# Kernel optimization log

Measured on AMD Instinct MI355X. Metric: run time of the kernel, lower is better.

Reference implementation:

```python
import jax, jax.numpy as jnp
import numpy as np
from jax import lax

B, T, VSZ = 32, 150, 500
EMB, HID, OSZ, VL, BETA = 80, 512, 512, 512, 512


def setup_inputs() -> dict:
    key = jax.random.key(0)
    ks = jax.random.split(key, 16)
    rn = lambda k, shp, s=0.02: jax.random.normal(k, shp, dtype=jnp.float32) * s
    return {
        "X_batch": jax.random.normal(ks[0], (B, 1, 64, 512), jnp.float32),
        "labels_batch": jax.random.randint(ks[1], (B, T), 0, VSZ),
        "w1": rn(ks[2], (64, 1, 3, 3)), "b1": jnp.zeros((64,), jnp.float32),
        "w2": rn(ks[3], (128, 64, 3, 3)), "b2": jnp.zeros((128,), jnp.float32),
        "w3": rn(ks[4], (256, 128, 3, 3)), "b3": jnp.zeros((256,), jnp.float32),
        "w4": rn(ks[5], (512, 256, 3, 3)), "b4": jnp.zeros((512,), jnp.float32),
        "E": rn(ks[6], (VSZ, EMB), 1.0),
        "Wx": rn(ks[7], (4 * HID, EMB + OSZ)),
        "Wh": rn(ks[8], (4 * HID, HID)),
        "b_lstm": jnp.zeros((4 * HID,), jnp.float32),
        "Wv_att": rn(ks[9], (VL, BETA)),
        "Wh_att": rn(ks[10], (HID, BETA)),
        "b_att": jnp.zeros((BETA,), jnp.float32),
        "beta_att": rn(ks[11], (BETA,)),
        "W_O": rn(ks[12], (OSZ, HID + VL)),
        "W_out": rn(ks[13], (VSZ, OSZ)),
    }


def _conv(x, w, b):
    y = lax.conv_general_dilated(x, w, (1, 1), 'SAME',
                                 dimension_numbers=('NCHW', 'OIHW', 'NCHW'))
    return y + b[None, :, None, None]


def _pool2(x):
    return lax.reduce_window(x, -jnp.inf, lax.max, (1, 1, 2, 2), (1, 1, 2, 2), 'VALID')


def _cnn(x, w1, b1, w2, b2, w3, b3, w4, b4):
    x = _pool2(jax.nn.relu(_conv(x, w1, b1)))   # (B,64,32,256)
    x = _pool2(jax.nn.relu(_conv(x, w2, b2)))   # (B,128,16,128)
    x = jax.nn.relu(_conv(x, w3, b3))           # (B,256,16,128)
    x = _pool2(jax.nn.relu(_conv(x, w4, b4)))   # (B,512,8,64)
    return x


def reference(X_batch, labels_batch, w1, b1, w2, b2, w3, b3, w4, b4,
              E, Wx, Wh, b_lstm, Wv_att, Wh_att, b_att, beta_att, W_O, W_out):
    f32 = X_batch.dtype
    bsz, seq = labels_batch.shape
    F = _cnn(X_batch, w1, b1, w2, b2, w3, b3, w4, b4)
    C = F.shape[1]
    V = F.transpose(0, 2, 3, 1).reshape(bsz, -1, C)        # (B, L=H'*W', C)
    Vproj = V @ Wv_att + b_att                              # (B, L, BETA) precomputed

    vocab = W_out.shape[0]
    start = jnp.full((bsz, 1), vocab - 3, labels_batch.dtype)
    ids = jnp.concatenate([start, labels_batch[:, :-1]], axis=1)  # teacher forcing
    embs = E[ids]                                           # (B, T, EMB)

    hid, osz = Wh.shape[1], W_O.shape[0]
    h0 = jnp.zeros((bsz, hid), f32)
    c0 = jnp.zeros((bsz, hid), f32)
    O0 = jnp.zeros((bsz, osz), f32)

    def step(carry, emb_t):
        h, c, O_prev = carry
        x = jnp.concatenate([emb_t, O_prev], axis=1)        # (B, EMB+OSZ)
        gates = x @ Wx.T + h @ Wh.T + b_lstm
        i_g, f_g, g_g, o_g = jnp.split(gates, 4, axis=1)
        c = jax.nn.sigmoid(f_g) * c + jax.nn.sigmoid(i_g) * jnp.tanh(g_g)
        h = jax.nn.sigmoid(o_g) * jnp.tanh(c)
        scores = jnp.tanh(Vproj + (h @ Wh_att)[:, None, :]) @ beta_att  # (B, L)
        a = jax.nn.softmax(scores, axis=-1)
        ctx = jnp.einsum('bl,blc->bc', a, V)                # (B, VL)
        O_t = jnp.tanh(jnp.concatenate([h, ctx], axis=1) @ W_O.T)
        Q_t = O_t @ W_out.T                                 # (B, vocab)
        return (h, c, O_t), Q_t

    _, Qs = lax.scan(step, (h0, c0, O0), embs.transpose(1, 0, 2))
    return Qs.transpose(1, 0, 2)                            # (B, T, vocab)
```

## Files before the change

kernel.cpp:

```cpp
#include <hip/hip_runtime.h>
#include <hip/hip_bf16.h>
#include <stdint.h>

typedef __attribute__((ext_vector_type(8))) short short8;
typedef __attribute__((ext_vector_type(4))) short short4v;
typedef __attribute__((ext_vector_type(4))) float f32x4;
using bf16 = __hip_bfloat16;

__device__ __forceinline__ float bfb2f(unsigned short u) {
  union { unsigned u; float f; } x; x.u = ((unsigned)u) << 16; return x.f;
}
__device__ __forceinline__ unsigned short f2bfb(float f) {
  union { float f; unsigned u; } x; x.f = f;
  unsigned r = x.u + 0x7FFFu + ((x.u >> 16) & 1u);
  return (unsigned short)(r >> 16);
}
__device__ __forceinline__ float sigf(float x) { return 1.0f / (1.0f + __expf(-x)); }
__device__ __forceinline__ float tanhf_(float x) {
  x = fminf(fmaxf(x, -15.f), 15.f);
  float e = __expf(2.f * x);
  return 1.f - 2.f / (e + 1.f);
}
__device__ __forceinline__ f32x4 mfma16(short8 a, short8 b, f32x4 c) {
  return __builtin_amdgcn_mfma_f32_16x16x32_bf16(a, b, c, 0, 0, 0);
}
__device__ __forceinline__ int swz(int b) { return b ^ (((b >> 6) & 7) << 4); }


__global__ void k_pack_apack(const float* __restrict__ w, bf16* __restrict__ out, int CO, int CI) {
  int idx = blockIdx.x * 256 + threadIdx.x;
  int total = 9 * CO * CI;
  if (idx >= total) return;
  int ci = idx % CI; int r = idx / CI; int co = r % CO; int s = r / CO;
  ((unsigned short*)out)[(s * CO + co) * CI + ci] = f2bfb(w[(co * CI + ci) * 9 + s]);
}

__global__ void k_cast(const float* __restrict__ src, bf16* __restrict__ dst, int n) {
  int idx = blockIdx.x * 256 + threadIdx.x;
  if (idx < n) ((unsigned short*)dst)[idx] = f2bfb(src[idx]);
}

__global__ void k_castT512(const float* __restrict__ src, bf16* __restrict__ dst) {
  int idx = blockIdx.x * 256 + threadIdx.x;
  if (idx >= 262144) return;
  int k = idx >> 9, nn = idx & 511;
  ((unsigned short*)dst)[nn * 512 + k] = f2bfb(src[idx]);
}

__global__ void k_pack_wg(const float* __restrict__ Wx, const float* __restrict__ Wh, bf16* __restrict__ out) {
  int idx = blockIdx.x * 256 + threadIdx.x;
  if (idx >= 2293760) return;
  int kj = idx & 7, jc = (idx >> 3) & 15; int r = idx >> 7;
  int kg = r % 140, jblk = r / 140;
  int k = kg * 8 + kj, j = jblk * 16 + jc;
  float v = 0.f;
  if (k < 80) v = Wx[j * 592 + k];
  else if (k < 96) v = 0.f;
  else if (k < 608) v = Wx[j * 592 + k - 16];
  else v = Wh[j * 512 + k - 608];
  ((unsigned short*)out)[idx] = f2bfb(v);
}
__global__ void k_pack_wo(const float* __restrict__ WO, bf16* __restrict__ out) {
  int idx = blockIdx.x * 256 + threadIdx.x;
  if (idx >= 524288) return;
  int kj = idx & 7, jc = (idx >> 3) & 15; int r = idx >> 7;
  int kg = r % 128, jblk = r / 128;
  int k = kg * 8 + kj, o = jblk * 16 + jc;
  ((unsigned short*)out)[idx] = f2bfb(WO[o * 1024 + k]);
}
__global__ void k_pack_wout(const float* __restrict__ W, bf16* __restrict__ out) {
  int idx = blockIdx.x * 256 + threadIdx.x;
  if (idx >= 262144) return;
  int kj = idx & 7, jc = (idx >> 3) & 15; int r = idx >> 7;
  int kg = r % 64, jblk = r / 64;
  int k = kg * 8 + kj, v = jblk * 16 + jc;
  ((unsigned short*)out)[idx] = (v < 500) ? f2bfb(W[v * 512 + k]) : (unsigned short)0;
}

__global__ void k_init(bf16* __restrict__ X, bf16* __restrict__ Hb, float* __restrict__ Cst,
                       const bf16* __restrict__ Ebf) {
  int idx = blockIdx.x * 256 + threadIdx.x;
  if (idx < 32 * 608) {
    int k = idx % 608;
    unsigned short v = 0;
    if (k < 80) v = ((const unsigned short*)Ebf)[497 * 80 + k];
    ((unsigned short*)X)[idx] = v;
  }
  if (idx < 32768) ((unsigned short*)Hb)[idx] = 0;
  if (idx < 16384) Cst[idx] = 0.f;
}


__global__ __launch_bounds__(256) void k_conv1(const float* __restrict__ Xin, const float* __restrict__ w1,
                                               const float* __restrict__ b1, bf16* __restrict__ out) {
  __shared__ float wsm[576];
  __shared__ float xt[4][10];
  const int tid = threadIdx.x;
  const int n = blockIdx.z, y2 = blockIdx.y, xb = blockIdx.x * 4;
  for (int i = tid; i < 576; i += 256) wsm[i] = w1[i];
  if (tid < 40) {
    int rr = tid / 10, cc = tid % 10;
    int gy = 2 * y2 - 1 + rr, gx = 2 * xb - 1 + cc;
    float v = 0.f;
    if (gy >= 0 && gy < 64 && gx >= 0 && gx < 512) v = Xin[n * 32768 + gy * 512 + gx];
    xt[rr][cc] = v;
  }
  __syncthreads();
  const int co = tid & 63, xl = tid >> 6;
  const float bb = b1[co];
  float mx = 0.f;
#pragma unroll
  for (int py = 0; py < 2; ++py)
#pragma unroll
    for (int px = 0; px < 2; ++px) {
      float s = bb;
#pragma unroll
      for (int dy = 0; dy < 3; ++dy)
#pragma unroll
        for (int dx = 0; dx < 3; ++dx)
          s = fmaf(wsm[co * 9 + dy * 3 + dx], xt[py + dy][2 * xl + px + dx], s);
      mx = fmaxf(mx, fmaxf(s, 0.f));
    }
  ((unsigned short*)out)[((n * 34 + y2 + 1) * 258 + (xb + xl) + 1) * 64 + co] = f2bfb(mx);
}

template <int CI, int CO, int H, int W, int MODE>
__global__ __launch_bounds__(256) void k_convgemm(const bf16* __restrict__ inP, const bf16* __restrict__ apack,
                                                  const float* __restrict__ bias, bf16* __restrict__ outp) {
  constexpr int Hp = H + 2, Wp = W + 2;
  __shared__ __align__(16) char As[8192];
  __shared__ __align__(16) char Bs[8192];
  const int tid = threadIdx.x, lane = tid & 63, wv = tid >> 6;
  const int lm = lane & 15, kh = lane >> 4;
  const int wm = wv & 1, wn = wv >> 1;
  const int p0 = blockIdx.x * 128, m0 = blockIdx.y * 128;
  const int n = p0 / (H * W), rem = p0 % (H * W);
  const int y = rem / W, x0 = rem % W;
  const long long pixbase = ((long long)(n * Hp + y) * Wp + x0) * CI;
  f32x4 acc[4][4];
#pragma unroll
  for (int i = 0; i < 4; ++i)
#pragma unroll
    for (int j = 0; j < 4; ++j) acc[i][j] = (f32x4){0.f, 0.f, 0.f, 0.f};
  const int r = tid >> 1, e0 = (tid & 1) * 16;
  const int wb = r * 64 + e0 * 2;
  for (int s = 0; s < 9; ++s) {
    const int dy = s / 3, dx = s % 3;
    const bf16* bsrc = inP + pixbase + (dy * Wp + dx) * CI;
    const bf16* asrc = apack + (s * CO + m0) * CI;
    for (int cc = 0; cc < CI / 32; ++cc) {
      short8 av0 = *(const short8*)(asrc + r * CI + cc * 32 + e0);
      short8 av1 = *(const short8*)(asrc + r * CI + cc * 32 + e0 + 8);
      short8 bv0 = *(const short8*)(bsrc + (long long)r * CI + cc * 32 + e0);
      short8 bv1 = *(const short8*)(bsrc + (long long)r * CI + cc * 32 + e0 + 8);
      __syncthreads();
      *(short8*)(void*)(As + swz(wb)) = av0;
      *(short8*)(void*)(As + swz(wb + 16)) = av1;
      *(short8*)(void*)(Bs + swz(wb)) = bv0;
      *(short8*)(void*)(Bs + swz(wb + 16)) = bv1;
      __syncthreads();
      short8 af[4], bg[4];
#pragma unroll
      for (int i = 0; i < 4; ++i)
        af[i] = *(const short8*)(const void*)(As + swz((wm * 64 + i * 16 + lm) * 64 + kh * 16));
#pragma unroll
      for (int j = 0; j < 4; ++j)
        bg[j] = *(const short8*)(const void*)(Bs + swz((wn * 64 + j * 16 + lm) * 64 + kh * 16));
#pragma unroll
      for (int i = 0; i < 4; ++i)
#pragma unroll
        for (int j = 0; j < 4; ++j) acc[i][j] = mfma16(af[i], bg[j], acc[i][j]);
    }
  }
#pragma unroll
  for (int i = 0; i < 4; ++i) {
    const int co = m0 + wm * 64 + i * 16 + kh * 4;
    float b4[4];
#pragma unroll
    for (int rr = 0; rr < 4; ++rr) b4[rr] = bias[co + rr];
#pragma unroll
    for (int j = 0; j < 4; ++j) {
      const int pix = p0 + wn * 64 + j * 16 + lm;
      short4v pk;
#pragma unroll
      for (int rr = 0; rr < 4; ++rr) {
        float v = fmaxf(acc[i][j][rr] + b4[rr], 0.f);
        pk[rr] = (short)f2bfb(v);
      }
      if constexpr (MODE == 0) {
        *(short4v*)(void*)(outp + (long long)pix * CO + co) = pk;
      } else {
        const int nn = pix / (H * W), r2 = pix % (H * W);
        const int yy = r2 / W, xx = r2 % W;
        *(short4v*)(void*)(outp + ((long long)(nn * Hp + yy + 1) * Wp + xx + 1) * CO + co) = pk;
      }
    }
  }
}

__global__ void k_pool(const bf16* __restrict__ src, bf16* __restrict__ dst,
                       int H, int W, int C, int OHP, int OWP, int pad) {
  const int idx = blockIdx.x * 256 + threadIdx.x;
  const int C8 = C >> 3;
  const int c8 = idx % C8; int tmp = idx / C8;
  const int x2 = tmp % (W >> 1); tmp /= (W >> 1);
  const int y2 = tmp % (H >> 1); const int n = tmp / (H >> 1);
  if (n >= 32) return;
  const long long sbase = ((long long)(n * H + 2 * y2) * W + 2 * x2) * C + c8 * 8;
  short8 a = *(const short8*)(src + sbase);
  short8 b = *(const short8*)(src + sbase + C);
  short8 c = *(const short8*)(src + sbase + (long long)W * C);
  short8 d = *(const short8*)(src + sbase + (long long)W * C + C);
  short8 o;
#pragma unroll
  for (int e = 0; e < 8; ++e) {
    float m = fmaxf(fmaxf(bfb2f((unsigned short)a[e]), bfb2f((unsigned short)b[e])),
                    fmaxf(bfb2f((unsigned short)c[e]), bfb2f((unsigned short)d[e])));
    o[e] = (short)f2bfb(m);
  }
  *(short8*)(void*)(dst + ((long long)(n * OHP + y2 + pad) * OWP + x2 + pad) * C + c8 * 8) = o;
}

__global__ __launch_bounds__(256) void k_gemm_vproj(const bf16* __restrict__ Vb, const bf16* __restrict__ WvT,
                                                    const float* __restrict__ batt, bf16* __restrict__ VP) {
  __shared__ __align__(16) char As[8192];
  __shared__ __align__(16) char Bs[8192];
  const int tid = threadIdx.x, lane = tid & 63, wv = tid >> 6;
  const int lm = lane & 15, kh = lane >> 4;
  const int wm = wv & 1, wn = wv >> 1;
  const int n0 = blockIdx.x * 128, m0 = blockIdx.y * 128;
  f32x4 acc[4][4];
#pragma unroll
  for (int i = 0; i < 4; ++i)
#pragma unroll
    for (int j = 0; j < 4; ++j) acc[i][j] = (f32x4){0.f, 0.f, 0.f, 0.f};
  const int r = tid >> 1, e0 = (tid & 1) * 16;
  const int wb = r * 64 + e0 * 2;
  for (int cc = 0; cc < 16; ++cc) {
    short8 av0 = *(const short8*)(Vb + (m0 + r) * 512 + cc * 32 + e0);
    short8 av1 = *(const short8*)(Vb + (m0 + r) * 512 + cc * 32 + e0 + 8);
    short8 bv0 = *(const short8*)(WvT + (n0 + r) * 512 + cc * 32 + e0);
    short8 bv1 = *(const short8*)(WvT + (n0 + r) * 512 + cc * 32 + e0 + 8);
    __syncthreads();
    *(short8*)(void*)(As + swz(wb)) = av0;
    *(short8*)(void*)(As + swz(wb + 16)) = av1;
    *(short8*)(void*)(Bs + swz(wb)) = bv0;
    *(short8*)(void*)(Bs + swz(wb + 16)) = bv1;
    __syncthreads();
    short8 af[4], bg[4];
#pragma unroll
    for (int i = 0; i < 4; ++i)
      af[i] = *(const short8*)(const void*)(As + swz((wm * 64 + i * 16 + lm) * 64 + kh * 16));
#pragma unroll
    for (int j = 0; j < 4; ++j)
      bg[j] = *(const short8*)(const void*)(Bs + swz((wn * 64 + j * 16 + lm) * 64 + kh * 16));
#pragma unroll
    for (int i = 0; i < 4; ++i)
#pragma unroll
      for (int j = 0; j < 4; ++j) acc[i][j] = mfma16(af[i], bg[j], acc[i][j]);
  }
#pragma unroll
  for (int i = 0; i < 4; ++i)
#pragma unroll
    for (int j = 0; j < 4; ++j) {
      const int nn = n0 + wn * 64 + j * 16 + lm;
      const float ba = batt[nn];
#pragma unroll
      for (int rr = 0; rr < 4; ++rr) {
        const int m = m0 + wm * 64 + i * 16 + kh * 4 + rr;
        ((unsigned short*)VP)[m * 512 + nn] = f2bfb(acc[i][j][rr] + ba);
      }
    }
}


__global__ __launch_bounds__(256) void k_step_a(int t, const bf16* __restrict__ X, bf16* __restrict__ Hb,
                                                float* __restrict__ Cst, const bf16* __restrict__ WgP,
                                                const bf16* __restrict__ WoutP, const float* __restrict__ bl,
                                                float* __restrict__ outQ) {
  const int tid = threadIdx.x, lane = tid & 63, wv = tid >> 6;
  const int lm = lane & 15, kh = lane >> 4;
  if (blockIdx.x < 32) {
    if (t >= 150) return;
    const int nb = blockIdx.x;
    const int jblk = wv * 32 + nb;
    const bf16* hprev = Hb + ((t + 1) & 1) * 16384;
    f32x4 acc0 = {0.f, 0.f, 0.f, 0.f}, acc1 = {0.f, 0.f, 0.f, 0.f};
    for (int kk = 0; kk < 19; ++kk) {
      short8 a0 = *(const short8*)(X + lm * 608 + kk * 32 + kh * 8);
      short8 a1 = *(const short8*)(X + (lm + 16) * 608 + kk * 32 + kh * 8);
      short8 b = *(const short8*)(WgP + ((jblk * 140 + kk * 4 + kh) * 16 + lm) * 8);
      acc0 = mfma16(a0, b, acc0);
      acc1 = mfma16(a1, b, acc1);
    }
    for (int kk = 19; kk < 35; ++kk) {
      short8 a0 = *(const short8*)(hprev + lm * 512 + (kk - 19) * 32 + kh * 8);
      short8 a1 = *(const short8*)(hprev + (lm + 16) * 512 + (kk - 19) * 32 + kh * 8);
      short8 b = *(const short8*)(WgP + ((jblk * 140 + kk * 4 + kh) * 16 + lm) * 8);
      acc0 = mfma16(a0, b, acc0);
      acc1 = mfma16(a1, b, acc1);
    }
    __shared__ float gl[4][32][16];
    const float bj = bl[wv * 512 + nb * 16 + lm];
#pragma unroll
    for (int rr = 0; rr < 4; ++rr) {
      gl[wv][kh * 4 + rr][lm] = acc0[rr] + bj;
      gl[wv][16 + kh * 4 + rr][lm] = acc1[rr] + bj;
    }
    __syncthreads();
    bf16* hcur = Hb + (t & 1) * 16384;
    for (int idx = tid; idx < 512; idx += 256) {
      const int b = idx >> 4, hh = idx & 15;
      const int hid = nb * 16 + hh;
      float ig = gl[0][b][hh], fg = gl[1][b][hh], gg = gl[2][b][hh], og = gl[3][b][hh];
      float c = sigf(fg) * Cst[b * 512 + hid] + sigf(ig) * tanhf_(gg);
      Cst[b * 512 + hid] = c;
      ((unsigned short*)hcur)[b * 512 + hid] = f2bfb(sigf(og) * tanhf_(c));
    }
  } else {
    if (t < 1) return;
    const int ntile = (blockIdx.x - 32) * 4 + wv;
    f32x4 acc0 = {0.f, 0.f, 0.f, 0.f}, acc1 = {0.f, 0.f, 0.f, 0.f};
    for (int kk = 0; kk < 16; ++kk) {
      short8 a0 = *(const short8*)(X + lm * 608 + 96 + kk * 32 + kh * 8);
      short8 a1 = *(const short8*)(X + (lm + 16) * 608 + 96 + kk * 32 + kh * 8);
      short8 b = *(const short8*)(WoutP + ((ntile * 64 + kk * 4 + kh) * 16 + lm) * 8);
      acc0 = mfma16(a0, b, acc0);
      acc1 = mfma16(a1, b, acc1);
    }
    const int v = ntile * 16 + lm;
    if (v < 500) {
#pragma unroll
      for (int rr = 0; rr < 4; ++rr) {
        outQ[((kh * 4 + rr) * 150 + (t - 1)) * 500 + v] = acc0[rr];
        outQ[((16 + kh * 4 + rr) * 150 + (t - 1)) * 500 + v] = acc1[rr];
      }
    }
  }
}

__global__ __launch_bounds__(256) void k_step_b(int t, const bf16* __restrict__ Hb,
                                                const bf16* __restrict__ WhattB, const bf16* __restrict__ Vproj,
                                                const float* __restrict__ beta, float* __restrict__ scores) {
  const int tid = threadIdx.x;
  const int b = blockIdx.x >> 2, lc = blockIdx.x & 3;
  __shared__ unsigned short hsh[512];
  __shared__ float hW[512];
  __shared__ float bsh[512];
  const unsigned short* hp = (const unsigned short*)(Hb + (t & 1) * 16384) + b * 512;
  for (int i = tid; i < 512; i += 256) {
    hsh[i] = hp[i];
    bsh[i] = beta[i];
  }
  __syncthreads();
  const uint32_t* wp = (const uint32_t*)WhattB;
  float s0 = 0.f, s1 = 0.f;
  for (int k = 0; k < 512; ++k) {
    const float hk = bfb2f(hsh[k]);
    const uint32_t w2 = wp[k * 256 + tid];
    s0 = fmaf(hk, bfb2f((unsigned short)(w2 & 0xFFFFu)), s0);
    s1 = fmaf(hk, bfb2f((unsigned short)(w2 >> 16)), s1);
  }
  hW[tid * 2] = s0;
  hW[tid * 2 + 1] = s1;
  __syncthreads();
  const int l = lc * 128 + (tid >> 1);
  const int half = tid & 1;
  const short8* vp = (const short8*)(Vproj + ((b * 512 + l) * 512) + half * 256);
  float acc = 0.f;
  for (int i = 0; i < 32; ++i) {
    short8 v = vp[i];
#pragma unroll
    for (int e = 0; e < 8; ++e) {
      const int be = half * 256 + i * 8 + e;
      acc = fmaf(tanhf_(bfb2f((unsigned short)v[e]) + hW[be]), bsh[be], acc);
    }
  }
  acc += __shfl_xor(acc, 1, 64);
  if (half == 0) scores[b * 512 + l] = acc;
}

__global__ __launch_bounds__(256) void k_step_c(const float* __restrict__ scores, const bf16* __restrict__ V,
                                                bf16* __restrict__ Ct) {
  const int tid = threadIdx.x;
  const int b = blockIdx.x >> 2, cc = blockIdx.x & 3;
  const int lane = tid & 63, wv = tid >> 6;
  __shared__ float sc[512];
  __shared__ float wr1[4];
  __shared__ float wr2[4];
  __shared__ float part[2][128];
  float v0 = scores[b * 512 + tid];
  float v1 = scores[b * 512 + 256 + tid];
  float m = fmaxf(v0, v1);
#pragma unroll
  for (int off = 32; off >= 1; off >>= 1) m = fmaxf(m, __shfl_xor(m, off, 64));
  if (lane == 0) wr1[wv] = m;
  __syncthreads();
  m = fmaxf(fmaxf(wr1[0], wr1[1]), fmaxf(wr1[2], wr1[3]));
  float e0 = __expf(v0 - m), e1 = __expf(v1 - m);
  sc[tid] = e0;
  sc[tid + 256] = e1;
  float s = e0 + e1;
#pragma unroll
  for (int off = 32; off >= 1; off >>= 1) s += __shfl_xor(s, off, 64);
  if (lane == 0) wr2[wv] = s;
  __syncthreads();
  const float rz = 1.0f / (wr2[0] + wr2[1] + wr2[2] + wr2[3]);
  const int c = cc * 128 + (tid & 127);
  const int lh = tid >> 7;
  const unsigned short* vb = (const unsigned short*)V + ((b * 512 + lh * 256) * 512) + c;
  float acc = 0.f;
  for (int l = 0; l < 256; ++l) acc = fmaf(sc[lh * 256 + l], bfb2f(vb[l * 512]), acc);
  part[lh][tid & 127] = acc;
  __syncthreads();
  if (tid < 128) ((unsigned short*)Ct)[b * 512 + cc * 128 + tid] = f2bfb((part[0][tid] + part[1][tid]) * rz);
}

__global__ __launch_bounds__(256) void k_step_d(int t, bf16* __restrict__ X, const bf16* __restrict__ Hb,
                                                const bf16* __restrict__ Ct, const bf16* __restrict__ WOP,
                                                const bf16* __restrict__ Ebf, const int* __restrict__ labels) {
  const int tid = threadIdx.x, lane = tid & 63, wv = tid >> 6;
  const int lm = lane & 15, kh = lane >> 4;
  const int ntile = blockIdx.x * 4 + wv;
  const bf16* hcur = Hb + (t & 1) * 16384;
  f32x4 acc0 = {0.f, 0.f, 0.f, 0.f}, acc1 = {0.f, 0.f, 0.f, 0.f};
  for (int kk = 0; kk < 16; ++kk) {
    short8 a0 = *(const short8*)(hcur + lm * 512 + kk * 32 + kh * 8);
    short8 a1 = *(const short8*)(hcur + (lm + 16) * 512 + kk * 32 + kh * 8);
    short8 b = *(const short8*)(WOP + ((ntile * 128 + kk * 4 + kh) * 16 + lm) * 8);
    acc0 = mfma16(a0, b, acc0);
    acc1 = mfma16(a1, b, acc1);
  }
  for (int kk = 16; kk < 32; ++kk) {
    short8 a0 = *(const short8*)(Ct + lm * 512 + (kk - 16) * 32 + kh * 8);
    short8 a1 = *(const short8*)(Ct + (lm + 16) * 512 + (kk - 16) * 32 + kh * 8);
    short8 b = *(const short8*)(WOP + ((ntile * 128 + kk * 4 + kh) * 16 + lm) * 8);
    acc0 = mfma16(a0, b, acc0);
    acc1 = mfma16(a1, b, acc1);
  }
  const int o = ntile * 16 + lm;
  unsigned short* Xu = (unsigned short*)X;
#pragma unroll
  for (int rr = 0; rr < 4; ++rr) {
    Xu[(kh * 4 + rr) * 608 + 96 + o] = f2bfb(tanhf_(acc0[rr]));
    Xu[(16 + kh * 4 + rr) * 608 + 96 + o] = f2bfb(tanhf_(acc1[rr]));
  }
  if (blockIdx.x == 0 && t + 1 < 150) {
    for (int idx = tid; idx < 3072; idx += 256) {
      const int b = idx / 96, k = idx % 96;
      unsigned short val = 0;
      if (k < 80) {
        const int id = labels[b * 150 + t];
        val = ((const unsigned short*)Ebf)[id * 80 + k];
      }
      Xu[b * 608 + k] = val;
    }
  }
}


extern "C" void kernel_launch(void* const* d_in, const int* in_sizes, int n_in,
                              void* d_out, int out_size, void* d_ws, size_t ws_size,
                              hipStream_t stream) {
  (void)in_sizes; (void)n_in; (void)out_size; (void)ws_size;
  const float* Xb = (const float*)d_in[0];
  const int* lab = (const int*)d_in[1];
  const float* w1 = (const float*)d_in[2]; const float* b1 = (const float*)d_in[3];
  const float* w2 = (const float*)d_in[4]; const float* b2 = (const float*)d_in[5];
  const float* w3 = (const float*)d_in[6]; const float* b3 = (const float*)d_in[7];
  const float* w4 = (const float*)d_in[8]; const float* b4 = (const float*)d_in[9];
  const float* E = (const float*)d_in[10];
  const float* Wx = (const float*)d_in[11]; const float* Wh = (const float*)d_in[12];
  const float* blstm = (const float*)d_in[13];
  const float* Wv = (const float*)d_in[14]; const float* Wha = (const float*)d_in[15];
  const float* bat = (const float*)d_in[16]; const float* beta = (const float*)d_in[17];
  const float* WO = (const float*)d_in[18]; const float* Wout = (const float*)d_in[19];
  float* out = (float*)d_out;
  char* ws = (char*)d_ws;

  constexpr size_t oRegA = 0;
  constexpr size_t sRegA = 38338560ULL;
  constexpr size_t oRegB = oRegA + sRegA;
  constexpr size_t oIn2p = oRegB + 67108864ULL;
  constexpr size_t oV    = oIn2p + 19169280ULL;
  constexpr size_t oVprj = oV + 16777216ULL;
  constexpr size_t oAp2  = oVprj + 16777216ULL;
  constexpr size_t oAp3  = oAp2 + 147456ULL;
  constexpr size_t oAp4  = oAp3 + 589824ULL;
  constexpr size_t oWvT  = oAp4 + 2359296ULL;
  constexpr size_t oWgP  = oWvT + 524288ULL;
  constexpr size_t oWOP  = oWgP + 4587520ULL;
  constexpr size_t oWoutP= oWOP + 1048576ULL;
  constexpr size_t oWhatt= oWoutP + 524288ULL;
  constexpr size_t oEbf  = oWhatt + 524288ULL;
  constexpr size_t oX    = oEbf + 80128ULL;
  constexpr size_t oHb   = oX + 39168ULL;
  constexpr size_t oCst  = oHb + 65536ULL;
  constexpr size_t oSc   = oCst + 65536ULL;
  constexpr size_t oCt   = oSc + 65536ULL;

  bf16* in1p = (bf16*)(ws + oRegA);
  bf16* in3p = (bf16*)(ws + oRegA);
  bf16* pre2 = (bf16*)(ws + oRegB);
  bf16* pre4 = (bf16*)(ws + oRegB);
  bf16* in2p = (bf16*)(ws + oIn2p);
  bf16* Vbuf = (bf16*)(ws + oV);
  bf16* Vprj = (bf16*)(ws + oVprj);
  bf16* Ap2 = (bf16*)(ws + oAp2);
  bf16* Ap3 = (bf16*)(ws + oAp3);
  bf16* Ap4 = (bf16*)(ws + oAp4);
  bf16* WvT = (bf16*)(ws + oWvT);
  bf16* WgP = (bf16*)(ws + oWgP);
  bf16* WOP = (bf16*)(ws + oWOP);
  bf16* WoutP = (bf16*)(ws + oWoutP);
  bf16* Whatt = (bf16*)(ws + oWhatt);
  bf16* Ebf = (bf16*)(ws + oEbf);
  bf16* X = (bf16*)(ws + oX);
  bf16* Hb = (bf16*)(ws + oHb);
  float* Cst = (float*)(ws + oCst);
  float* Sc = (float*)(ws + oSc);
  bf16* Ct = (bf16*)(ws + oCt);

  k_pack_apack<<<(9 * 128 * 64 + 255) / 256, 256, 0, stream>>>(w2, Ap2, 128, 64);
  k_pack_apack<<<(9 * 256 * 128 + 255) / 256, 256, 0, stream>>>(w3, Ap3, 256, 128);
  k_pack_apack<<<(9 * 512 * 256 + 255) / 256, 256, 0, stream>>>(w4, Ap4, 512, 256);
  k_castT512<<<1024, 256, 0, stream>>>(Wv, WvT);
  k_cast<<<1024, 256, 0, stream>>>(Wha, Whatt, 262144);
  k_cast<<<(40000 + 255) / 256, 256, 0, stream>>>(E, Ebf, 40000);
  k_pack_wg<<<8960, 256, 0, stream>>>(Wx, Wh, WgP);
  k_pack_wo<<<2048, 256, 0, stream>>>(WO, WOP);
  k_pack_wout<<<1024, 256, 0, stream>>>(Wout, WoutP);
  k_init<<<128, 256, 0, stream>>>(X, Hb, Cst, Ebf);

  hipMemsetAsync(ws + oRegA, 0, sRegA, stream);
  hipMemsetAsync(ws + oIn2p, 0, 19169280ULL, stream);
  k_conv1<<<dim3(64, 32, 32), 256, 0, stream>>>(Xb, w1, b1, in1p);
  k_convgemm<64, 128, 32, 256, 0><<<dim3(2048, 1), 256, 0, stream>>>(in1p, Ap2, b2, pre2);
  k_pool<<<4096, 256, 0, stream>>>(pre2, in2p, 32, 256, 128, 18, 130, 1);
  hipMemsetAsync(ws + oRegA, 0, sRegA, stream);
  k_convgemm<128, 256, 16, 128, 1><<<dim3(512, 2), 256, 0, stream>>>(in2p, Ap3, b3, in3p);
  k_convgemm<256, 512, 16, 128, 0><<<dim3(512, 4), 256, 0, stream>>>(in3p, Ap4, b4, pre4);
  k_pool<<<4096, 256, 0, stream>>>(pre4, Vbuf, 16, 128, 512, 8, 64, 0);
  k_gemm_vproj<<<dim3(4, 128), 256, 0, stream>>>(Vbuf, WvT, bat, Vprj);

  for (int t = 0; t <= 150; ++t) {
    k_step_a<<<40, 256, 0, stream>>>(t, X, Hb, Cst, WgP, WoutP, blstm, out);
    if (t == 150) break;
    k_step_b<<<128, 256, 0, stream>>>(t, Hb, Whatt, Vprj, beta, Sc);
    k_step_c<<<128, 256, 0, stream>>>(Sc, Vbuf, Ct);
    k_step_d<<<8, 256, 0, stream>>>(t, X, Hb, Ct, WOP, Ebf, lab);
  }
}
```

Measured before the change: 11.99 ms.

## Fuse decoder timestep loop into one persistent kernel with grid barriers

Replaces the roughly 600 per-step kernel launches of the 151-step decoder with a single persistent 256-block kernel that uses an atomic grid barrier between phases. The cell state is kept in registers. The h@Wh_att product is folded into the LSTM blocks as MFMA partial sums, which are reduced in the scores phase. h and the attention context are packed into one buffer so the W_O matmul reads a single contiguous operand. The intent is to remove launch overhead and poorly parallelised small kernels, at the cost of relying on all 256 blocks being co-resident and on spin-barrier latency.

```diff
diff --git a/kernel.cpp b/kernel.cpp
--- a/kernel.cpp
+++ b/kernel.cpp
@@ -25,6 +25,23 @@
   return __builtin_amdgcn_mfma_f32_16x16x32_bf16(a, b, c, 0, 0, 0);
 }
 __device__ __forceinline__ int swz(int b) { return b ^ (((b >> 6) & 7) << 4); }
+
+__device__ __forceinline__ void gbar(int* cnt, int* gen, int target) {
+  __syncthreads();
+  if (threadIdx.x == 0) {
+    int v = __hip_atomic_fetch_add(cnt, 1, __ATOMIC_ACQ_REL, __HIP_MEMORY_SCOPE_AGENT);
+    if (v == 255) {
+      __hip_atomic_store(cnt, 0, __ATOMIC_RELAXED, __HIP_MEMORY_SCOPE_AGENT);
+      __hip_atomic_fetch_add(gen, 1, __ATOMIC_ACQ_REL, __HIP_MEMORY_SCOPE_AGENT);
+    } else {
+      while (__hip_atomic_load(gen, __ATOMIC_RELAXED, __HIP_MEMORY_SCOPE_AGENT) < target) {
+        __builtin_amdgcn_s_sleep(1);
+      }
+      __builtin_amdgcn_fence(__ATOMIC_ACQUIRE, "agent");
+    }
+  }
+  __syncthreads();
+}
 
 
 __global__ void k_pack_apack(const float* __restrict__ w, bf16* __restrict__ out, int CO, int CI) {
@@ -76,9 +93,15 @@
   int k = kg * 8 + kj, v = jblk * 16 + jc;
   ((unsigned short*)out)[idx] = (v < 500) ? f2bfb(W[v * 512 + k]) : (unsigned short)0;
 }
-
-__global__ void k_init(bf16* __restrict__ X, bf16* __restrict__ Hb, float* __restrict__ Cst,
-                       const bf16* __restrict__ Ebf) {
+__global__ void k_pack_whatt(const float* __restrict__ Wha, bf16* __restrict__ out) {
+  int idx = blockIdx.x * 256 + threadIdx.x;
+  if (idx >= 262144) return;
+  int kj = idx & 7, jc = (idx >> 3) & 15, khh = (idx >> 7) & 1, j2 = (idx >> 8) & 31, nb = idx >> 13;
+  int k = nb * 16 + khh * 8 + kj, n = j2 * 16 + jc;
+  ((unsigned short*)out)[idx] = f2bfb(Wha[k * 512 + n]);
+}
+
+__global__ void k_init(bf16* __restrict__ X, bf16* __restrict__ HC, const bf16* __restrict__ Ebf) {
   int idx = blockIdx.x * 256 + threadIdx.x;
   if (idx < 32 * 608) {
     int k = idx % 608;
@@ -86,8 +109,7 @@
     if (k < 80) v = ((const unsigned short*)Ebf)[497 * 80 + k];
     ((unsigned short*)X)[idx] = v;
   }
-  if (idx < 32768) ((unsigned short*)Hb)[idx] = 0;
-  if (idx < 16384) Cst[idx] = 0.f;
+  if (idx < 65536) ((unsigned short*)HC)[idx] = 0;
 }
 
 
@@ -273,187 +295,192 @@
     }
 }
 
-
-__global__ __launch_bounds__(256) void k_step_a(int t, const bf16* __restrict__ X, bf16* __restrict__ Hb,
-                                                float* __restrict__ Cst, const bf16* __restrict__ WgP,
-                                                const bf16* __restrict__ WoutP, const float* __restrict__ bl,
-                                                float* __restrict__ outQ) {
-  const int tid = threadIdx.x, lane = tid & 63, wv = tid >> 6;
-  const int lm = lane & 15, kh = lane >> 4;
-  if (blockIdx.x < 32) {
-    if (t >= 150) return;
-    const int nb = blockIdx.x;
-    const int jblk = wv * 32 + nb;
-    const bf16* hprev = Hb + ((t + 1) & 1) * 16384;
-    f32x4 acc0 = {0.f, 0.f, 0.f, 0.f}, acc1 = {0.f, 0.f, 0.f, 0.f};
-    for (int kk = 0; kk < 19; ++kk) {
-      short8 a0 = *(const short8*)(X + lm * 608 + kk * 32 + kh * 8);
-      short8 a1 = *(const short8*)(X + (lm + 16) * 608 + kk * 32 + kh * 8);
-      short8 b = *(const short8*)(WgP + ((jblk * 140 + kk * 4 + kh) * 16 + lm) * 8);
-      acc0 = mfma16(a0, b, acc0);
-      acc1 = mfma16(a1, b, acc1);
-    }
-    for (int kk = 19; kk < 35; ++kk) {
-      short8 a0 = *(const short8*)(hprev + lm * 512 + (kk - 19) * 32 + kh * 8);
-      short8 a1 = *(const short8*)(hprev + (lm + 16) * 512 + (kk - 19) * 32 + kh * 8);
-      short8 b = *(const short8*)(WgP + ((jblk * 140 + kk * 4 + kh) * 16 + lm) * 8);
-      acc0 = mfma16(a0, b, acc0);
-      acc1 = mfma16(a1, b, acc1);
-    }
-    __shared__ float gl[4][32][16];
-    const float bj = bl[wv * 512 + nb * 16 + lm];
-#pragma unroll
-    for (int rr = 0; rr < 4; ++rr) {
-      gl[wv][kh * 4 + rr][lm] = acc0[rr] + bj;
-      gl[wv][16 + kh * 4 + rr][lm] = acc1[rr] + bj;
-    }
-    __syncthreads();
-    bf16* hcur = Hb + (t & 1) * 16384;
-    for (int idx = tid; idx < 512; idx += 256) {
-      const int b = idx >> 4, hh = idx & 15;
-      const int hid = nb * 16 + hh;
-      float ig = gl[0][b][hh], fg = gl[1][b][hh], gg = gl[2][b][hh], og = gl[3][b][hh];
-      float c = sigf(fg) * Cst[b * 512 + hid] + sigf(ig) * tanhf_(gg);
-      Cst[b * 512 + hid] = c;
-      ((unsigned short*)hcur)[b * 512 + hid] = f2bfb(sigf(og) * tanhf_(c));
-    }
-  } else {
-    if (t < 1) return;
-    const int ntile = (blockIdx.x - 32) * 4 + wv;
-    f32x4 acc0 = {0.f, 0.f, 0.f, 0.f}, acc1 = {0.f, 0.f, 0.f, 0.f};
-    for (int kk = 0; kk < 16; ++kk) {
-      short8 a0 = *(const short8*)(X + lm * 608 + 96 + kk * 32 + kh * 8);
-      short8 a1 = *(const short8*)(X + (lm + 16) * 608 + 96 + kk * 32 + kh * 8);
-      short8 b = *(const short8*)(WoutP + ((ntile * 64 + kk * 4 + kh) * 16 + lm) * 8);
-      acc0 = mfma16(a0, b, acc0);
-      acc1 = mfma16(a1, b, acc1);
-    }
-    const int v = ntile * 16 + lm;
-    if (v < 500) {
+__global__ __launch_bounds__(256) void k_decoder(
+    bf16* __restrict__ X, bf16* __restrict__ HC, float* __restrict__ partial,
+    float* __restrict__ scores, const bf16* __restrict__ WgP, const bf16* __restrict__ WhattP,
+    const bf16* __restrict__ WOP, const bf16* __restrict__ WoutP,
+    const bf16* __restrict__ Vprj, const bf16* __restrict__ Vbuf,
+    const bf16* __restrict__ Ebf, const int* __restrict__ labels,
+    const float* __restrict__ bl, const float* __restrict__ beta,
+    float* __restrict__ out, int* syncp) {
+  const int tid = threadIdx.x, bid = blockIdx.x;
+  const int lane = tid & 63, wv = tid >> 6, lm = lane & 15, kh = lane >> 4;
+  __shared__ __align__(16) char smem[12288];
+  int* cnt = syncp;
+  int* gen = syncp + 32;
+  int bt = 0;
+  float c0 = 0.f, c1 = 0.f;
+  const short8 z8 = {0, 0, 0, 0, 0, 0, 0, 0};
+  const f32x4 z4 = {0.f, 0.f, 0.f, 0.f};
+  unsigned short* Xu = (unsigned short*)X;
+  unsigned short* HCu = (unsigned short*)HC;
+
+  for (int t = 0; t < 151; ++t) {
+    gbar(cnt, gen, ++bt);
+    if (bid < 32 && t < 150) {
+      const int nb = bid;
+      const bf16* hprev = HC + ((t + 1) & 1) * 32768;
+      const int jblk = wv * 32 + nb;
+      f32x4 acc0 = z4, acc1 = z4;
+      for (int kk = 0; kk < 19; ++kk) {
+        short8 a0 = *(const short8*)(X + lm * 608 + kk * 32 + kh * 8);
+        short8 a1 = *(const short8*)(X + (lm + 16) * 608 + kk * 32 + kh * 8);
+        short8 bw = *(const short8*)(WgP + ((jblk * 140 + kk * 4 + kh) * 16 + lm) * 8);
+        acc0 = mfma16(a0, bw, acc0); acc1 = mfma16(a1, bw, acc1);
+      }
+      for (int kk = 19; kk < 35; ++kk) {
+        short8 a0 = *(const short8*)(hprev + lm * 1024 + (kk - 19) * 32 + kh * 8);
+        short8 a1 = *(const short8*)(hprev + (lm + 16) * 1024 + (kk - 19) * 32 + kh * 8);
+        short8 bw = *(const short8*)(WgP + ((jblk * 140 + kk * 4 + kh) * 16 + lm) * 8);
+        acc0 = mfma16(a0, bw, acc0); acc1 = mfma16(a1, bw, acc1);
+      }
+      float* gl = (float*)smem;
+      unsigned short* hsl = (unsigned short*)(smem + 8192);
+      const float bj = bl[wv * 512 + nb * 16 + lm];
 #pragma unroll
       for (int rr = 0; rr < 4; ++rr) {
-        outQ[((kh * 4 + rr) * 150 + (t - 1)) * 500 + v] = acc0[rr];
-        outQ[((16 + kh * 4 + rr) * 150 + (t - 1)) * 500 + v] = acc1[rr];
-      }
-    }
-  }
-}
-
-__global__ __launch_bounds__(256) void k_step_b(int t, const bf16* __restrict__ Hb,
-                                                const bf16* __restrict__ WhattB, const bf16* __restrict__ Vproj,
-                                                const float* __restrict__ beta, float* __restrict__ scores) {
-  const int tid = threadIdx.x;
-  const int b = blockIdx.x >> 2, lc = blockIdx.x & 3;
-  __shared__ unsigned short hsh[512];
-  __shared__ float hW[512];
-  __shared__ float bsh[512];
-  const unsigned short* hp = (const unsigned short*)(Hb + (t & 1) * 16384) + b * 512;
-  for (int i = tid; i < 512; i += 256) {
-    hsh[i] = hp[i];
-    bsh[i] = beta[i];
-  }
-  __syncthreads();
-  const uint32_t* wp = (const uint32_t*)WhattB;
-  float s0 = 0.f, s1 = 0.f;
-  for (int k = 0; k < 512; ++k) {
-    const float hk = bfb2f(hsh[k]);
-    const uint32_t w2 = wp[k * 256 + tid];
-    s0 = fmaf(hk, bfb2f((unsigned short)(w2 & 0xFFFFu)), s0);
-    s1 = fmaf(hk, bfb2f((unsigned short)(w2 >> 16)), s1);
-  }
-  hW[tid * 2] = s0;
-  hW[tid * 2 + 1] = s1;
-  __syncthreads();
-  const int l = lc * 128 + (tid >> 1);
-  const int half = tid & 1;
-  const short8* vp = (const short8*)(Vproj + ((b * 512 + l) * 512) + half * 256);
-  float acc = 0.f;
-  for (int i = 0; i < 32; ++i) {
-    short8 v = vp[i];
-#pragma unroll
-    for (int e = 0; e < 8; ++e) {
-      const int be = half * 256 + i * 8 + e;
-      acc = fmaf(tanhf_(bfb2f((unsigned short)v[e]) + hW[be]), bsh[be], acc);
-    }
-  }
-  acc += __shfl_xor(acc, 1, 64);
-  if (half == 0) scores[b * 512 + l] = acc;
-}
-
-__global__ __launch_bounds__(256) void k_step_c(const float* __restrict__ scores, const bf16* __restrict__ V,
-                                                bf16* __restrict__ Ct) {
-  const int tid = threadIdx.x;
-  const int b = blockIdx.x >> 2, cc = blockIdx.x & 3;
-  const int lane = tid & 63, wv = tid >> 6;
-  __shared__ float sc[512];
-  __shared__ float wr1[4];
-  __shared__ float wr2[4];
-  __shared__ float part[2][128];
-  float v0 = scores[b * 512 + tid];
-  float v1 = scores[b * 512 + 256 + tid];
-  float m = fmaxf(v0, v1);
-#pragma unroll
-  for (int off = 32; off >= 1; off >>= 1) m = fmaxf(m, __shfl_xor(m, off, 64));
-  if (lane == 0) wr1[wv] = m;
-  __syncthreads();
-  m = fmaxf(fmaxf(wr1[0], wr1[1]), fmaxf(wr1[2], wr1[3]));
-  float e0 = __expf(v0 - m), e1 = __expf(v1 - m);
-  sc[tid] = e0;
-  sc[tid + 256] = e1;
-  float s = e0 + e1;
-#pragma unroll
-  for (int off = 32; off >= 1; off >>= 1) s += __shfl_xor(s, off, 64);
-  if (lane == 0) wr2[wv] = s;
-  __syncthreads();
-  const float rz = 1.0f / (wr2[0] + wr2[1] + wr2[2] + wr2[3]);
-  const int c = cc * 128 + (tid & 127);
-  const int lh = tid >> 7;
-  const unsigned short* vb = (const unsigned short*)V + ((b * 512 + lh * 256) * 512) + c;
-  float acc = 0.f;
-  for (int l = 0; l < 256; ++l) acc = fmaf(sc[lh * 256 + l], bfb2f(vb[l * 512]), acc);
-  part[lh][tid & 127] = acc;
-  __syncthreads();
-  if (tid < 128) ((unsigned short*)Ct)[b * 512 + cc * 128 + tid] = f2bfb((part[0][tid] + part[1][tid]) * rz);
-}
-
-__global__ __launch_bounds__(256) void k_step_d(int t, bf16* __restrict__ X, const bf16* __restrict__ Hb,
-                                                const bf16* __restrict__ Ct, const bf16* __restrict__ WOP,
-                                                const bf16* __restrict__ Ebf, const int* __restrict__ labels) {
-  const int tid = threadIdx.x, lane = tid & 63, wv = tid >> 6;
-  const int lm = lane & 15, kh = lane >> 4;
-  const int ntile = blockIdx.x * 4 + wv;
-  const bf16* hcur = Hb + (t & 1) * 16384;
-  f32x4 acc0 = {0.f, 0.f, 0.f, 0.f}, acc1 = {0.f, 0.f, 0.f, 0.f};
-  for (int kk = 0; kk < 16; ++kk) {
-    short8 a0 = *(const short8*)(hcur + lm * 512 + kk * 32 + kh * 8);
-    short8 a1 = *(const short8*)(hcur + (lm + 16) * 512 + kk * 32 + kh * 8);
-    short8 b = *(const short8*)(WOP + ((ntile * 128 + kk * 4 + kh) * 16 + lm) * 8);
-    acc0 = mfma16(a0, b, acc0);
-    acc1 = mfma16(a1, b, acc1);
-  }
-  for (int kk = 16; kk < 32; ++kk) {
-    short8 a0 = *(const short8*)(Ct + lm * 512 + (kk - 16) * 32 + kh * 8);
-    short8 a1 = *(const short8*)(Ct + (lm + 16) * 512 + (kk - 16) * 32 + kh * 8);
-    short8 b = *(const short8*)(WOP + ((ntile * 128 + kk * 4 + kh) * 16 + lm) * 8);
-    acc0 = mfma16(a0, b, acc0);
-    acc1 = mfma16(a1, b, acc1);
-  }
-  const int o = ntile * 16 + lm;
-  unsigned short* Xu = (unsigned short*)X;
-#pragma unroll
-  for (int rr = 0; rr < 4; ++rr) {
-    Xu[(kh * 4 + rr) * 608 + 96 + o] = f2bfb(tanhf_(acc0[rr]));
-    Xu[(16 + kh * 4 + rr) * 608 + 96 + o] = f2bfb(tanhf_(acc1[rr]));
-  }
-  if (blockIdx.x == 0 && t + 1 < 150) {
-    for (int idx = tid; idx < 3072; idx += 256) {
-      const int b = idx / 96, k = idx % 96;
-      unsigned short val = 0;
-      if (k < 80) {
-        const int id = labels[b * 150 + t];
-        val = ((const unsigned short*)Ebf)[id * 80 + k];
-      }
-      Xu[b * 608 + k] = val;
+        gl[(wv * 32 + kh * 4 + rr) * 16 + lm] = acc0[rr] + bj;
+        gl[(wv * 32 + 16 + kh * 4 + rr) * 16 + lm] = acc1[rr] + bj;
+      }
+      __syncthreads();
+      unsigned short* hcur = HCu + (t & 1) * 32768;
+      {
+        const int b = tid >> 4, hh = tid & 15;
+        float ig = gl[(0 * 32 + b) * 16 + hh], fg = gl[(1 * 32 + b) * 16 + hh];
+        float gg = gl[(2 * 32 + b) * 16 + hh], og = gl[(3 * 32 + b) * 16 + hh];
+        c0 = sigf(fg) * c0 + sigf(ig) * tanhf_(gg);
+        unsigned short hv = f2bfb(sigf(og) * tanhf_(c0));
+        hcur[b * 1024 + nb * 16 + hh] = hv; hsl[b * 16 + hh] = hv;
+        const int b2 = 16 + b;
+        float ig2 = gl[(0 * 32 + b2) * 16 + hh], fg2 = gl[(1 * 32 + b2) * 16 + hh];
+        float gg2 = gl[(2 * 32 + b2) * 16 + hh], og2 = gl[(3 * 32 + b2) * 16 + hh];
+        c1 = sigf(fg2) * c1 + sigf(ig2) * tanhf_(gg2);
+        unsigned short hv2 = f2bfb(sigf(og2) * tanhf_(c1));
+        hcur[b2 * 1024 + nb * 16 + hh] = hv2; hsl[b2 * 16 + hh] = hv2;
+      }
+      __syncthreads();
+      short8 a0 = z8, a1 = z8;
+      if (kh < 2) {
+        a0 = *(const short8*)(hsl + lm * 16 + kh * 8);
+        a1 = *(const short8*)(hsl + (16 + lm) * 16 + kh * 8);
+      }
+      for (int j2 = wv * 8; j2 < wv * 8 + 8; ++j2) {
+        short8 bw = z8;
+        if (kh < 2) bw = *(const short8*)(WhattP + (((nb * 32 + j2) * 2 + kh) * 16 + lm) * 8);
+        f32x4 p0 = mfma16(a0, bw, z4);
+        f32x4 p1 = mfma16(a1, bw, z4);
+        float* pw = partial + nb * 16384 + j2 * 16 + lm;
+#pragma unroll
+        for (int rr = 0; rr < 4; ++rr) {
+          pw[(kh * 4 + rr) * 512] = p0[rr];
+          pw[(16 + kh * 4 + rr) * 512] = p1[rr];
+        }
+      }
+    } else if (bid >= 32 && bid < 40 && t >= 1) {
+      const int ntile = (bid - 32) * 4 + wv;
+      f32x4 acc0 = z4, acc1 = z4;
+      for (int kk = 0; kk < 16; ++kk) {
+        short8 a0 = *(const short8*)(X + lm * 608 + 96 + kk * 32 + kh * 8);
+        short8 a1 = *(const short8*)(X + (lm + 16) * 608 + 96 + kk * 32 + kh * 8);
+        short8 bw = *(const short8*)(WoutP + ((ntile * 64 + kk * 4 + kh) * 16 + lm) * 8);
+        acc0 = mfma16(a0, bw, acc0); acc1 = mfma16(a1, bw, acc1);
+      }
+      const int v = ntile * 16 + lm;
+      if (v < 500) {
+#pragma unroll
+        for (int rr = 0; rr < 4; ++rr) {
+          out[((kh * 4 + rr) * 150 + (t - 1)) * 500 + v] = acc0[rr];
+          out[((16 + kh * 4 + rr) * 150 + (t - 1)) * 500 + v] = acc1[rr];
+        }
+      }
+    }
+    if (t == 150) break;
+
+    gbar(cnt, gen, ++bt);
+    {
+      const int b = bid >> 3, chunk = bid & 7;
+      float* hWl = (float*)smem;
+      float* betal = (float*)(smem + 2048);
+      for (int n = tid; n < 512; n += 256) {
+        float s = 0.f;
+#pragma unroll 8
+        for (int nb = 0; nb < 32; ++nb) s += partial[nb * 16384 + b * 512 + n];
+        hWl[n] = s;
+        betal[n] = beta[n];
+      }
+      __syncthreads();
+      const int l = chunk * 64 + (tid >> 2), q = tid & 3;
+      const bf16* vp = Vprj + (b * 512 + l) * 512 + q * 128;
+      float acc = 0.f;
+      for (int i = 0; i < 16; ++i) {
+        short8 v = *(const short8*)(vp + i * 8);
+#pragma unroll
+        for (int e = 0; e < 8; ++e) {
+          const int n = q * 128 + i * 8 + e;
+          acc = fmaf(tanhf_(bfb2f((unsigned short)v[e]) + hWl[n]), betal[n], acc);
+        }
+      }
+      acc += __shfl_xor(acc, 1, 64);
+      acc += __shfl_xor(acc, 2, 64);
+      if (q == 0) scores[b * 512 + l] = acc;
+    }
+
+    gbar(cnt, gen, ++bt);
+    {
+      const int b = bid >> 3, cc = bid & 7;
+      float* al = (float*)smem;
+      float* prt = (float*)(smem + 2048);
+      float* wr = (float*)(smem + 3072);
+      float s0 = scores[b * 512 + tid], s1 = scores[b * 512 + 256 + tid];
+      float m = fmaxf(s0, s1);
+#pragma unroll
+      for (int off = 32; off >= 1; off >>= 1) m = fmaxf(m, __shfl_xor(m, off, 64));
+      if (lane == 0) wr[wv] = m;
+      __syncthreads();
+      m = fmaxf(fmaxf(wr[0], wr[1]), fmaxf(wr[2], wr[3]));
+      float e0 = __expf(s0 - m), e1 = __expf(s1 - m);
+      al[tid] = e0; al[tid + 256] = e1;
+      float s = e0 + e1;
+#pragma unroll
+      for (int off = 32; off >= 1; off >>= 1) s += __shfl_xor(s, off, 64);
+      if (lane == 0) wr[4 + wv] = s;
+      __syncthreads();
+      const float rz = 1.f / (wr[4] + wr[5] + wr[6] + wr[7]);
+      const int c = cc * 64 + (tid & 63), lq = tid >> 6;
+      const unsigned short* vb = (const unsigned short*)Vbuf + (long long)(b * 512 + lq * 128) * 512 + c;
+      float acc = 0.f;
+      for (int l = 0; l < 128; ++l) acc = fmaf(al[lq * 128 + l], bfb2f(vb[l * 512]), acc);
+      prt[lq * 64 + (tid & 63)] = acc;
+      __syncthreads();
+      if (tid < 64)
+        HCu[(t & 1) * 32768 + b * 1024 + 512 + cc * 64 + tid] =
+            f2bfb((prt[tid] + prt[64 + tid] + prt[128 + tid] + prt[192 + tid]) * rz);
+    }
+
+    gbar(cnt, gen, ++bt);
+    if (bid < 8) {
+      const int w = bid * 4 + wv;
+      const bf16* hc = HC + (t & 1) * 32768;
+      f32x4 acc0 = z4, acc1 = z4;
+      for (int kk = 0; kk < 32; ++kk) {
+        short8 a0 = *(const short8*)(hc + lm * 1024 + kk * 32 + kh * 8);
+        short8 a1 = *(const short8*)(hc + (lm + 16) * 1024 + kk * 32 + kh * 8);
+        short8 bw = *(const short8*)(WOP + ((w * 128 + kk * 4 + kh) * 16 + lm) * 8);
+        acc0 = mfma16(a0, bw, acc0); acc1 = mfma16(a1, bw, acc1);
+      }
+      const int o = w * 16 + lm;
+#pragma unroll
+      for (int rr = 0; rr < 4; ++rr) {
+        Xu[(kh * 4 + rr) * 608 + 96 + o] = f2bfb(tanhf_(acc0[rr]));
+        Xu[(16 + kh * 4 + rr) * 608 + 96 + o] = f2bfb(tanhf_(acc1[rr]));
+      }
+    } else if (bid == 8 && t + 1 < 150) {
+      for (int idx = tid; idx < 3072; idx += 256) {
+        const int b = idx / 96, k = idx % 96;
+        unsigned short val = 0;
+        if (k < 80) val = ((const unsigned short*)Ebf)[labels[b * 150 + t] * 80 + k];
+        Xu[b * 608 + k] = val;
+      }
     }
   }
 }
@@ -491,13 +518,13 @@
   constexpr size_t oWgP  = oWvT + 524288ULL;
   constexpr size_t oWOP  = oWgP + 4587520ULL;
   constexpr size_t oWoutP= oWOP + 1048576ULL;
-  constexpr size_t oWhatt= oWoutP + 524288ULL;
-  constexpr size_t oEbf  = oWhatt + 524288ULL;
-  constexpr size_t oX    = oEbf + 80128ULL;
-  constexpr size_t oHb   = oX + 39168ULL;
-  constexpr size_t oCst  = oHb + 65536ULL;
-  constexpr size_t oSc   = oCst + 65536ULL;
-  constexpr size_t oCt   = oSc + 65536ULL;
+  constexpr size_t oWhatP= oWoutP + 524288ULL;
+  constexpr size_t oEbf  = oWhatP + 524288ULL;
+  constexpr size_t oX    = oRegB;
+  constexpr size_t oHC   = oRegB + 39168ULL;
+  constexpr size_t oPart = oRegB + 170240ULL;
+  constexpr size_t oScr  = oRegB + 2267392ULL;
+  constexpr size_t oSync = oRegB + 2332928ULL;
 
   bf16* in1p = (bf16*)(ws + oRegA);
   bf16* in3p = (bf16*)(ws + oRegA);
@@ -513,24 +540,22 @@
   bf16* WgP = (bf16*)(ws + oWgP);
   bf16* WOP = (bf16*)(ws + oWOP);
   bf16* WoutP = (bf16*)(ws + oWoutP);
-  bf16* Whatt = (bf16*)(ws + oWhatt);
+  bf16* WhattP = (bf16*)(ws + oWhatP);
   bf16* Ebf = (bf16*)(ws + oEbf);
   bf16* X = (bf16*)(ws + oX);
-  bf16* Hb = (bf16*)(ws + oHb);
-  float* Cst = (float*)(ws + oCst);
-  float* Sc = (float*)(ws + oSc);
-  bf16* Ct = (bf16*)(ws + oCt);
+  bf16* HC = (bf16*)(ws + oHC);
+  float* Part = (float*)(ws + oPart);
+  float* Scr = (float*)(ws + oScr);
 
   k_pack_apack<<<(9 * 128 * 64 + 255) / 256, 256, 0, stream>>>(w2, Ap2, 128, 64);
   k_pack_apack<<<(9 * 256 * 128 + 255) / 256, 256, 0, stream>>>(w3, Ap3, 256, 128);
   k_pack_apack<<<(9 * 512 * 256 + 255) / 256, 256, 0, stream>>>(w4, Ap4, 512, 256);
   k_castT512<<<1024, 256, 0, stream>>>(Wv, WvT);
-  k_cast<<<1024, 256, 0, stream>>>(Wha, Whatt, 262144);
   k_cast<<<(40000 + 255) / 256, 256, 0, stream>>>(E, Ebf, 40000);
   k_pack_wg<<<8960, 256, 0, stream>>>(Wx, Wh, WgP);
   k_pack_wo<<<2048, 256, 0, stream>>>(WO, WOP);
   k_pack_wout<<<1024, 256, 0, stream>>>(Wout, WoutP);
-  k_init<<<128, 256, 0, stream>>>(X, Hb, Cst, Ebf);
+  k_pack_whatt<<<1024, 256, 0, stream>>>(Wha, WhattP);
 
   hipMemsetAsync(ws + oRegA, 0, sRegA, stream);
   hipMemsetAsync(ws + oIn2p, 0, 19169280ULL, stream);
@@ -543,11 +568,9 @@
   k_pool<<<4096, 256, 0, stream>>>(pre4, Vbuf, 16, 128, 512, 8, 64, 0);
   k_gemm_vproj<<<dim3(4, 128), 256, 0, stream>>>(Vbuf, WvT, bat, Vprj);
 
-  for (int t = 0; t <= 150; ++t) {
-    k_step_a<<<40, 256, 0, stream>>>(t, X, Hb, Cst, WgP, WoutP, blstm, out);
-    if (t == 150) break;
-    k_step_b<<<128, 256, 0, stream>>>(t, Hb, Whatt, Vprj, beta, Sc);
-    k_step_c<<<128, 256, 0, stream>>>(Sc, Vbuf, Ct);
-    k_step_d<<<8, 256, 0, stream>>>(t, X, Hb, Ct, WOP, Ebf, lab);
-  }
-}
+  k_init<<<256, 256, 0, stream>>>(X, HC, Ebf);
+  hipMemsetAsync(ws + oSync, 0, 256, stream);
+  k_decoder<<<256, 256, 0, stream>>>(X, HC, Part, Scr, WgP, WhattP, WOP, WoutP,
+                                     Vprj, Vbuf, Ebf, lab, blstm, beta, out,
+                                     (int*)(ws + oSync));
+}
```

After: 17.78 ms. 48.3% more time.
